# Kernel optimization log

Measured on AMD Instinct MI355X. Metric: run time of the kernel, lower is better.

Reference implementation:

```python
import jax, jax.numpy as jnp
import numpy as np

BATCH, T, HID = 4, 2048, 1024
H = P = 1024  # input_dim and ssm_size (expand_ratio=1.0)
EPS = 1e-5
DISCRETIZATION = "IM"  # 'IM' or 'IMEX'


def setup_inputs() -> dict:
    key = jax.random.key(0)
    ks = jax.random.split(key, 10)
    std_b = 1.0 / np.sqrt(H)
    std_c = 1.0 / np.sqrt(P)
    u = lambda k, s, lo, hi: jax.random.uniform(k, s, jnp.float32, lo, hi)
    return {
        "hidden_states": jax.random.normal(ks[0], (BATCH, T, HID), jnp.float32),
        "Wi": jax.random.normal(ks[1], (H, HID), jnp.float32) / np.sqrt(HID),
        "Wg": jax.random.normal(ks[2], (H, HID), jnp.float32) / np.sqrt(HID),
        "Wo": jax.random.normal(ks[3], (HID, H), jnp.float32) / np.sqrt(H),
        "A_diag": u(ks[4], (P,), 0.0, 1.0),
        "B_param": u(ks[5], (P, H, 2), -std_b, std_b),
        "C_param": u(ks[6], (H, P, 2), -std_c, std_c),
        "D": jax.random.normal(ks[7], (H,), jnp.float32),
        "dt": u(ks[8], (P,), 0.0, 1.0),
        "norm_weight": jnp.ones((H,), jnp.float32),
    }


def _linoss(x, B_param, C_param, A_diag, dt_p, D):
    """LinOSS oscillatory SSM recurrence with complex B/C and diagonal A.
    x: (B,T,H) real input. State z,y in C^P (re/im stacked on last axis)."""
    A = jax.nn.relu(A_diag)       # (P,) nonneg frequencies
    dt = jax.nn.sigmoid(dt_p)     # (P,) timesteps in (0,1)
    # Bu_{re,im}[b,t,p] = sum_h x[b,t,h] * B_{re,im}[p,h]
    Bu = jnp.einsum('bth,phc->btpc', x, B_param)  # (B,T,P,2)
    if DISCRETIZATION == "IM":
        S = 1.0 / (1.0 + dt * dt * A)
        m11, m12, m21, m22 = S, -dt * A * S, dt * S, S
        f1, f2 = dt * S, dt * dt * S
    else:  # IMEX
        one = jnp.ones_like(dt)
        m11, m12, m21, m22 = one, -dt * A, dt, 1.0 - dt * dt * A
        f1, f2 = dt, dt * dt
    c = lambda v: v[None, :, None]  # broadcast (P,) -> (B,P,2)

    def step(carry, bu):
        z, y = carry  # each (B,P,2)
        z1 = c(m11) * z + c(m12) * y + c(f1) * bu
        y1 = c(m21) * z + c(m22) * y + c(f2) * bu
        return (z1, y1), y1

    z0 = jnp.zeros((x.shape[0], A.shape[0], 2), x.dtype)
    _, ys = jax.lax.scan(step, (z0, z0), jnp.swapaxes(Bu, 0, 1))
    ys = jnp.swapaxes(ys, 0, 1)  # (B,T,P,2)
    # o = Re(C @ y) + D * x
    o = (jnp.einsum('btp,hp->bth', ys[..., 0], C_param[..., 0])
         - jnp.einsum('btp,hp->bth', ys[..., 1], C_param[..., 1]))
    return o + x * D


def reference(hidden_states, Wi, Wg, Wo, A_diag, B_param, C_param, D, dt, norm_weight):
    x = hidden_states @ Wi.T                        # i_proj
    o = _linoss(x, B_param, C_param, A_diag, dt, D)  # fused_recurrent_linoss
    g = hidden_states @ Wg.T                        # g_proj
    # FusedRMSNormGated: rmsnorm(o) * weight * swish(g)
    o = o * jax.lax.rsqrt(jnp.mean(o * o, axis=-1, keepdims=True) + EPS) * norm_weight
    o = o * (g * jax.nn.sigmoid(g))
    return o @ Wo.T                                  # o_proj
```

## Files before the change

kernel.cpp:

```cpp
#include <hip/hip_runtime.h>
#include <hip/hip_bf16.h>
#include <math.h>

#define BB 4
#define TT 2048
#define HH 1024
#define PP 1024
#define MT 8192
#define C2 2048
#define NC 64
#define LCH 32

typedef __attribute__((ext_vector_type(8))) short  bf16x8;
typedef __attribute__((ext_vector_type(4))) float  f32x4;

__device__ __forceinline__ ushort f2bf(float f) {
    union { float f; unsigned u; } v; v.f = f;
    unsigned r = v.u + 0x7fffu + ((v.u >> 16) & 1u);
    return (ushort)(r >> 16);
}
__device__ __forceinline__ float bf2f(ushort h) {
    union { unsigned u; float f; } v; v.u = ((unsigned)h) << 16;
    return v.f;
}

__device__ __forceinline__ void gload16(const ushort* g, ushort* l) {
    __builtin_amdgcn_global_load_lds((const __attribute__((address_space(1))) void*)g,
                                     (__attribute__((address_space(3))) void*)l,
                                     16, 0, 0);
}
__device__ __forceinline__ void barrier_raw() { __builtin_amdgcn_s_barrier(); }
__device__ __forceinline__ void lgk0() { asm volatile("s_waitcnt lgkmcnt(0)" ::: "memory"); }
__device__ __forceinline__ void vm6()  { asm volatile("s_waitcnt vmcnt(6)"   ::: "memory"); }
__device__ __forceinline__ void vm0()  { asm volatile("s_waitcnt vmcnt(0)"   ::: "memory"); }

__global__ void convert_all(const float* __restrict__ hs, const float* __restrict__ Wi,
                            const float* __restrict__ Wg, const float* __restrict__ Wo,
                            ushort* __restrict__ hsb, ushort* __restrict__ Wigb,
                            ushort* __restrict__ Wob) {
    int i = blockIdx.x * 256 + threadIdx.x;
    const int HS4 = MT * HH / 4;
    const int W4  = HH * HH / 4;
    const float4* s;
    ushort4* d;
    if (i < HS4)               { s = (const float4*)hs + i;               d = (ushort4*)hsb  + i; }
    else if (i < HS4 + 2 * W4) { int j = i - HS4;
                                 s = (const float4*)(j < W4 ? Wi : Wg) + (j < W4 ? j : j - W4);
                                 d = (ushort4*)Wigb + j; }
    else                       { int j = i - HS4 - 2 * W4;
                                 s = (const float4*)Wo + j;               d = (ushort4*)Wob + j; }
    float4 v = *s;
    ushort4 o;
    o.x = f2bf(v.x); o.y = f2bf(v.y); o.z = f2bf(v.z); o.w = f2bf(v.w);
    *d = o;
}

__global__ void repack_B_bf(const float* __restrict__ src, ushort* __restrict__ dst) {
    int idx = blockIdx.x * 256 + threadIdx.x;
    int p = idx >> 10;
    int h = idx & 1023;
    float2 v = ((const float2*)src)[idx];
    dst[(size_t)p * HH + h]        = f2bf(v.x);
    dst[(size_t)(p + PP) * HH + h] = f2bf(v.y);
}

__global__ void repack_C_bf(const float* __restrict__ src, ushort* __restrict__ dst) {
    int idx = blockIdx.x * 256 + threadIdx.x;
    int h = idx >> 10;
    int p = idx & 1023;
    float2 v = ((const float2*)src)[idx];
    dst[(size_t)h * C2 + p]      = f2bf(v.x);
    dst[(size_t)h * C2 + PP + p] = f2bf(-v.y);
}

template<int BM, int STORE_BF16>
__global__ __launch_bounds__(512, 2) void gemm8p(
    const ushort* __restrict__ A, int lda,
    const ushort* __restrict__ B, int ldb,
    void* __restrict__ Cp, int ldc, int K, int nbx)
{
    constexpr int BN  = 256;
    constexpr int MR  = BM / 32;
    constexpr int MRH = MR / 2;
    constexpr int TA  = BM * 128;
    constexpr int TB  = BN * 128;
    __shared__ __align__(16) char smem[2 * TA + 2 * TB];

    const int bid = blockIdx.x;
    const int cpx = gridDim.x >> 3;
    const int wg  = (bid & 7) * cpx + (bid >> 3);
    const int by  = wg / nbx;
    const int bx  = wg - by * nbx;
    const int bm  = by * BM;
    const int bn  = bx * BN;

    const int tid  = threadIdx.x;
    const int wave = tid >> 6;
    const int lane = tid & 63;
    const int wr   = wave >> 2;
    const int wc   = wave & 3;
    const int lr   = lane & 15;
    const int kg   = lane >> 4;

    const int e  = (wave << 10) + ((lane << 4) ^ (((lane >> 3) & 7) << 4));
    const int r0 = e >> 7;
    const int c0 = (e & 127) >> 1;

    auto stA = [&](int bi, int u, int kt) {
        gload16(A + (size_t)(bm + u * 64 + r0) * lda + kt * 64 + c0,
                (ushort*)(smem + bi * TA + u * 8192 + (wave << 10)));
    };
    auto stB = [&](int bi, int u, int kt) {
        gload16(B + (size_t)(bn + u * 64 + r0) * ldb + kt * 64 + c0,
                (ushort*)(smem + 2 * TA + bi * TB + u * 8192 + (wave << 10)));
    };

    bf16x8 Af[MRH][2], Bf[4][2];
    auto ldsA = [&](int bi, int qm) {
#pragma unroll
        for (int f = 0; f < MRH; ++f)
#pragma unroll
            for (int kk = 0; kk < 2; ++kk) {
                int row = wr * (BM / 2) + qm * (BM / 4) + f * 16 + lr;
                int o = row * 128 + kk * 64 + kg * 16;
                o ^= (row & 7) << 4;
                Af[f][kk] = *(const bf16x8*)(smem + bi * TA + o);
            }
    };
    auto ldsB = [&](int bi) {
#pragma unroll
        for (int n = 0; n < 4; ++n)
#pragma unroll
            for (int kk = 0; kk < 2; ++kk) {
                int row = wc * 64 + n * 16 + lr;
                int o = row * 128 + kk * 64 + kg * 16;
                o ^= (row & 7) << 4;
                Bf[n][kk] = *(const bf16x8*)(smem + 2 * TA + bi * TB + o);
            }
    };

    f32x4 acc[MR][4];
#pragma unroll
    for (int m = 0; m < MR; ++m)
#pragma unroll
        for (int n = 0; n < 4; ++n)
#pragma unroll
            for (int i = 0; i < 4; ++i) acc[m][n][i] = 0.f;

    auto mfma16 = [&](int qm, int qn) {
        __builtin_amdgcn_s_setprio(1);
#pragma unroll
        for (int f = 0; f < MRH; ++f)
#pragma unroll
            for (int n2 = 0; n2 < 2; ++n2)
#pragma unroll
                for (int kk = 0; kk < 2; ++kk)
                    acc[qm * MRH + f][qn * 2 + n2] =
                        __builtin_amdgcn_mfma_f32_16x16x32_bf16(
                            Af[f][kk], Bf[qn * 2 + n2][kk],
                            acc[qm * MRH + f][qn * 2 + n2], 0, 0, 0);
        __builtin_amdgcn_s_setprio(0);
    };

    if constexpr (BM == 256) {
        stA(0, 0, 0); stA(0, 1, 0); stA(0, 2, 0); stA(0, 3, 0);
        stB(0, 0, 0); stB(0, 1, 0); stB(0, 2, 0); stB(0, 3, 0);
        stB(1, 0, 1); stB(1, 1, 1); stB(1, 2, 1); stB(1, 3, 1);
        stA(1, 0, 1); stA(1, 2, 1);
    } else {
        stA(0, 0, 0); stA(0, 1, 0);
        stB(0, 0, 0); stB(0, 1, 0); stB(0, 2, 0); stB(0, 3, 0);
        stA(1, 0, 1); stA(1, 1, 1);
        stB(1, 0, 1); stB(1, 1, 1); stB(1, 2, 1); stB(1, 3, 1);
    }
    vm6();
    barrier_raw();

    const int nIter = K >> 7;
    for (int J = 0; J < nIter; ++J) {
        const bool pf  = (J + 1 < nIter);
        const int  kt1 = 2 * J + 1, kt2 = 2 * J + 2, kt3 = 2 * J + 3;
        ldsA(0, 0); ldsB(0);
        if constexpr (BM == 256) { stA(1, 1, kt1); stA(1, 3, kt1); }
        barrier_raw(); lgk0(); mfma16(0, 0); barrier_raw();
        if (pf) { stB(0, 0, kt2); stB(0, 1, kt2); }
        barrier_raw(); lgk0(); mfma16(0, 1); barrier_raw();
        ldsA(0, 1);
        if (pf) { stB(0, 2, kt2); stB(0, 3, kt2); }
        barrier_raw(); lgk0(); mfma16(1, 0); barrier_raw();
        if (pf) {
            if constexpr (BM == 256) { stA(0, 0, kt2); stA(0, 2, kt2); }
            else                     { stA(0, 0, kt2); stA(0, 1, kt2); }
        }
        barrier_raw(); lgk0(); mfma16(1, 1);
        if (pf) vm6(); else vm0();
        barrier_raw();
        ldsA(1, 0); ldsB(1);
        if constexpr (BM == 256) { if (pf) { stA(0, 1, kt2); stA(0, 3, kt2); } }
        barrier_raw(); lgk0(); mfma16(0, 0); barrier_raw();
        if (pf) { stB(1, 0, kt3); stB(1, 1, kt3); }
        barrier_raw(); lgk0(); mfma16(0, 1); barrier_raw();
        ldsA(1, 1);
        if (pf) { stB(1, 2, kt3); stB(1, 3, kt3); }
        barrier_raw(); lgk0(); mfma16(1, 0); barrier_raw();
        if (pf) {
            if constexpr (BM == 256) { stA(1, 0, kt3); stA(1, 2, kt3); }
            else                     { stA(1, 0, kt3); stA(1, 1, kt3); }
        }
        barrier_raw(); lgk0(); mfma16(1, 1);
        if (pf) vm6(); else vm0();
        barrier_raw();
    }

#pragma unroll
    for (int mf = 0; mf < MR; ++mf) {
#pragma unroll
        for (int n = 0; n < 4; ++n) {
            int col = bn + wc * 64 + n * 16 + lr;
#pragma unroll
            for (int i = 0; i < 4; ++i) {
                int row = bm + wr * (BM / 2) + mf * 16 + kg * 4 + i;
                float v = acc[mf][n][i];
                if (STORE_BF16)
                    ((ushort*)Cp)[(size_t)row * ldc + col] = f2bf(v);
                else
                    ((float*)Cp)[(size_t)row * ldc + col]  = v;
            }
        }
    }
}

__device__ __forceinline__ void linoss_coeffs(const float* A_diag, const float* dt_p,
                                              int p, float& m11, float& m12,
                                              float& m21, float& m22,
                                              float& f1, float& f2) {
    float A  = fmaxf(A_diag[p], 0.f);
    float dt = 1.f / (1.f + expf(-dt_p[p]));
    float S  = 1.f / (1.f + dt * dt * A);
    m11 = S;        m12 = -dt * A * S;
    m21 = dt * S;   m22 = S;
    f1  = dt * S;   f2  = dt * dt * S;
}

__global__ void scan_passA(const ushort* __restrict__ Bu,
                           const float* __restrict__ A_diag,
                           const float* __restrict__ dt_p,
                           float2* __restrict__ sEnd) {
    int c = blockIdx.x * 256 + threadIdx.x;
    int b = blockIdx.y;
    int j = blockIdx.z;
    float m11, m12, m21, m22, f1, f2;
    linoss_coeffs(A_diag, dt_p, c & 1023, m11, m12, m21, m22, f1, f2);
    const ushort* bu = Bu + ((size_t)(b * TT + j * LCH)) * C2 + c;
    float z = 0.f, y = 0.f;
#pragma unroll 8
    for (int i = 0; i < LCH; ++i) {
        float u  = bf2f(bu[(size_t)i * C2]);
        float z1 = m11 * z + m12 * y + f1 * u;
        float y1 = m21 * z + m22 * y + f2 * u;
        z = z1; y = y1;
    }
    sEnd[((size_t)j * BB + b) * C2 + c] = make_float2(z, y);
}

__global__ void scan_combine(const float* __restrict__ A_diag,
                             const float* __restrict__ dt_p,
                             const float2* __restrict__ sEnd,
                             float2* __restrict__ sInit) {
    int idx = blockIdx.x * 256 + threadIdx.x;
    int c = idx & (C2 - 1);
    int b = idx >> 11;
    float m11, m12, m21, m22, f1, f2;
    linoss_coeffs(A_diag, dt_p, c & 1023, m11, m12, m21, m22, f1, f2);
    float e11 = m11, e12 = m12, e21 = m21, e22 = m22;
#pragma unroll
    for (int s = 0; s < 5; ++s) {
        float n11 = e11 * e11 + e12 * e21;
        float n12 = e11 * e12 + e12 * e22;
        float n21 = e21 * e11 + e22 * e21;
        float n22 = e21 * e12 + e22 * e22;
        e11 = n11; e12 = n12; e21 = n21; e22 = n22;
    }
    float z = 0.f, y = 0.f;
    for (int j = 0; j < NC; ++j) {
        size_t off = ((size_t)j * BB + b) * C2 + c;
        sInit[off] = make_float2(z, y);
        float2 le = sEnd[off];
        float z1 = e11 * z + e12 * y + le.x;
        float y1 = e21 * z + e22 * y + le.y;
        z = z1; y = y1;
    }
}

__global__ void scan_passB(const ushort* __restrict__ Bu,
                           const float* __restrict__ A_diag,
                           const float* __restrict__ dt_p,
                           const float2* __restrict__ sInit,
                           ushort* __restrict__ YSb) {
    int c = blockIdx.x * 256 + threadIdx.x;
    int b = blockIdx.y;
    int j = blockIdx.z;
    float m11, m12, m21, m22, f1, f2;
    linoss_coeffs(A_diag, dt_p, c & 1023, m11, m12, m21, m22, f1, f2);
    float2 s0 = sInit[((size_t)j * BB + b) * C2 + c];
    float z = s0.x, y = s0.y;
    const ushort* bu = Bu  + ((size_t)(b * TT + j * LCH)) * C2 + c;
    ushort*       ys = YSb + ((size_t)(b * TT + j * LCH)) * C2 + c;
#pragma unroll 8
    for (int i = 0; i < LCH; ++i) {
        float u  = bf2f(bu[(size_t)i * C2]);
        float z1 = m11 * z + m12 * y + f1 * u;
        float y1 = m21 * z + m22 * y + f2 * u;
        z = z1; y = y1;
        ys[(size_t)i * C2] = f2bf(y);
    }
}

__global__ void rmsgate_kernel(const float* __restrict__ O,
                               const ushort* __restrict__ XGb,
                               const float* __restrict__ Dv,
                               const float* __restrict__ nw,
                               ushort* __restrict__ V) {
    int m = blockIdx.x;
    int t = threadIdx.x;
    float4  o4 = ((const float4*)(O + (size_t)m * HH))[t];
    ushort4 x4 = ((const ushort4*)(XGb + (size_t)m * C2))[t];
    float4  d4 = ((const float4*)Dv)[t];
    float of[4];
    of[0] = o4.x + d4.x * bf2f(x4.x);
    of[1] = o4.y + d4.y * bf2f(x4.y);
    of[2] = o4.z + d4.z * bf2f(x4.z);
    of[3] = o4.w + d4.w * bf2f(x4.w);
    float ss = of[0]*of[0] + of[1]*of[1] + of[2]*of[2] + of[3]*of[3];
#pragma unroll
    for (int o = 32; o > 0; o >>= 1) ss += __shfl_down(ss, o);
    __shared__ float wsum[4];
    if ((t & 63) == 0) wsum[t >> 6] = ss;
    __syncthreads();
    float tot = wsum[0] + wsum[1] + wsum[2] + wsum[3];
    float r = rsqrtf(tot * (1.f / (float)HH) + 1e-5f);

    ushort4 g4 = ((const ushort4*)(XGb + (size_t)m * C2 + HH))[t];
    float4  w4 = ((const float4*)nw)[t];
    float g[4] = {bf2f(g4.x), bf2f(g4.y), bf2f(g4.z), bf2f(g4.w)};
    float w[4] = {w4.x, w4.y, w4.z, w4.w};
    ushort4 vout;
    ushort* vo = &vout.x;
#pragma unroll
    for (int i = 0; i < 4; ++i) {
        float sw = g[i] / (1.f + expf(-g[i]));
        vo[i] = f2bf(of[i] * r * w[i] * sw);
    }
    ((ushort4*)(V + (size_t)m * HH))[t] = vout;
}

extern "C" void kernel_launch(void* const* d_in, const int* in_sizes, int n_in,
                              void* d_out, int out_size, void* d_ws, size_t ws_size,
                              hipStream_t stream) {
    const float* hs      = (const float*)d_in[0];
    const float* Wi      = (const float*)d_in[1];
    const float* Wg      = (const float*)d_in[2];
    const float* Wo      = (const float*)d_in[3];
    const float* A_diag  = (const float*)d_in[4];
    const float* B_param = (const float*)d_in[5];
    const float* C_param = (const float*)d_in[6];
    const float* Dv      = (const float*)d_in[7];
    const float* dtp     = (const float*)d_in[8];
    const float* nw      = (const float*)d_in[9];
    float* out = (float*)d_out;

    char* ws = (char*)d_ws;
    ushort* hsb  = (ushort*)ws;                                   ws += (size_t)MT * HH * 2;
    ushort* Wigb = (ushort*)ws;                                   ws += (size_t)C2 * HH * 2;
    ushort* Wob  = (ushort*)ws;                                   ws += (size_t)HH * HH * 2;
    ushort* Bpkb = (ushort*)ws;                                   ws += (size_t)C2 * HH * 2;
    ushort* Cpkb = (ushort*)ws;                                   ws += (size_t)HH * C2 * 2;
    ushort* XGb  = (ushort*)ws;                                   ws += (size_t)MT * C2 * 2;
    ushort* Bu   = (ushort*)ws;                                   ws += (size_t)MT * C2 * 2;
    ushort* YSb  = (ushort*)ws;                                   ws += (size_t)MT * C2 * 2;
    float*  O    = (float*)ws;                                    ws += (size_t)MT * HH * 4;
    ushort* Vb   = (ushort*)ws;                                   ws += (size_t)MT * HH * 2;
    float2* sEnd  = (float2*)ws;                                  ws += (size_t)NC * BB * C2 * 8;
    float2* sInit = (float2*)ws;

    dim3 blk(256);

    convert_all<<<dim3((MT * HH / 4 + 3 * HH * HH / 4) / 256), blk, 0, stream>>>(
        hs, Wi, Wg, Wo, hsb, Wigb, Wob);
    repack_B_bf<<<dim3((PP * HH) / 256), blk, 0, stream>>>(B_param, Bpkb);
    repack_C_bf<<<dim3((HH * PP) / 256), blk, 0, stream>>>(C_param, Cpkb);

    gemm8p<256, 1><<<dim3(256), dim3(512), 0, stream>>>(
        hsb, HH, Wigb, HH, XGb, C2, HH, 8);

    gemm8p<256, 1><<<dim3(256), dim3(512), 0, stream>>>(
        XGb, C2, Bpkb, HH, Bu, C2, HH, 8);

    scan_passA<<<dim3(C2 / 256, BB, NC), blk, 0, stream>>>(Bu, A_diag, dtp, sEnd);
    scan_combine<<<dim3((BB * C2) / 256), blk, 0, stream>>>(A_diag, dtp, sEnd, sInit);
    scan_passB<<<dim3(C2 / 256, BB, NC), blk, 0, stream>>>(Bu, A_diag, dtp, sInit, YSb);

    gemm8p<128, 0><<<dim3(256), dim3(512), 0, stream>>>(
        YSb, C2, Cpkb, C2, O, HH, C2, 4);

    rmsgate_kernel<<<dim3(MT), blk, 0, stream>>>(O, XGb, Dv, nw, Vb);

    gemm8p<128, 0><<<dim3(256), dim3(512), 0, stream>>>(
        Vb, HH, Wob, HH, out, HH, HH, 4);
}
```

Before: 196.5 us.

## Add 4-phase pipelined 128x256 GEMM for output projections and store O in bf16

```diff
diff --git a/kernel.cpp b/kernel.cpp
--- a/kernel.cpp
+++ b/kernel.cpp
@@ -31,6 +31,7 @@
 }
 __device__ __forceinline__ void barrier_raw() { __builtin_amdgcn_s_barrier(); }
 __device__ __forceinline__ void lgk0() { asm volatile("s_waitcnt lgkmcnt(0)" ::: "memory"); }
+__device__ __forceinline__ void vm4()  { asm volatile("s_waitcnt vmcnt(4)"   ::: "memory"); }
 __device__ __forceinline__ void vm6()  { asm volatile("s_waitcnt vmcnt(6)"   ::: "memory"); }
 __device__ __forceinline__ void vm0()  { asm volatile("s_waitcnt vmcnt(0)"   ::: "memory"); }
 
@@ -220,6 +221,148 @@
 #pragma unroll
             for (int i = 0; i < 4; ++i) {
                 int row = bm + wr * (BM / 2) + mf * 16 + kg * 4 + i;
+                float v = acc[mf][n][i];
+                if (STORE_BF16)
+                    ((ushort*)Cp)[(size_t)row * ldc + col] = f2bf(v);
+                else
+                    ((float*)Cp)[(size_t)row * ldc + col]  = v;
+            }
+        }
+    }
+}
+
+template<int STORE_BF16>
+__global__ __launch_bounds__(512, 2) void gemm4p(
+    const ushort* __restrict__ A, int lda,
+    const ushort* __restrict__ B, int ldb,
+    void* __restrict__ Cp, int ldc, int K, int nbx)
+{
+    constexpr int BM = 128, BN = 256;
+    constexpr int TA = BM * 128;
+    constexpr int TB = BN * 128;
+    __shared__ __align__(16) char smem[2 * TA + 2 * TB];
+
+    const int bid = blockIdx.x;
+    const int cpx = gridDim.x >> 3;
+    const int wg  = (bid & 7) * cpx + (bid >> 3);
+    const int by  = wg / nbx;
+    const int bx  = wg - by * nbx;
+    const int bm  = by * BM;
+    const int bn  = bx * BN;
+
+    const int tid  = threadIdx.x;
+    const int wave = tid >> 6;
+    const int lane = tid & 63;
+    const int wr   = wave >> 2;
+    const int wc   = wave & 3;
+    const int lr   = lane & 15;
+    const int kg   = lane >> 4;
+
+    const int e  = (wave << 10) + ((lane << 4) ^ (((lane >> 3) & 7) << 4));
+    const int r0 = e >> 7;
+    const int c0 = (e & 127) >> 1;
+
+    auto stA = [&](int bi, int u, int kt) {
+        gload16(A + (size_t)(bm + u * 64 + r0) * lda + kt * 64 + c0,
+                (ushort*)(smem + bi * TA + u * 8192 + (wave << 10)));
+    };
+    auto stB = [&](int bi, int u, int kt) {
+        gload16(B + (size_t)(bn + u * 64 + r0) * ldb + kt * 64 + c0,
+                (ushort*)(smem + 2 * TA + bi * TB + u * 8192 + (wave << 10)));
+    };
+
+    bf16x8 Af[2][2], Bf[4][2];
+    auto ldsA = [&](int bi, int qm) {
+#pragma unroll
+        for (int f = 0; f < 2; ++f)
+#pragma unroll
+            for (int kk = 0; kk < 2; ++kk) {
+                int row = wr * 64 + qm * 32 + f * 16 + lr;
+                int o = row * 128 + kk * 64 + kg * 16;
+                o ^= (row & 7) << 4;
+                Af[f][kk] = *(const bf16x8*)(smem + bi * TA + o);
+            }
+    };
+    auto ldsB = [&](int bi) {
+#pragma unroll
+        for (int n = 0; n < 4; ++n)
+#pragma unroll
+            for (int kk = 0; kk < 2; ++kk) {
+                int row = wc * 64 + n * 16 + lr;
+                int o = row * 128 + kk * 64 + kg * 16;
+                o ^= (row & 7) << 4;
+                Bf[n][kk] = *(const bf16x8*)(smem + 2 * TA + bi * TB + o);
+            }
+    };
+
+    f32x4 acc[4][4];
+#pragma unroll
+    for (int m = 0; m < 4; ++m)
+#pragma unroll
+        for (int n = 0; n < 4; ++n)
+#pragma unroll
+            for (int i = 0; i < 4; ++i) acc[m][n][i] = 0.f;
+
+    auto cl = [&](int qm) {
+        __builtin_amdgcn_s_setprio(1);
+#pragma unroll
+        for (int f = 0; f < 2; ++f)
+#pragma unroll
+            for (int n = 0; n < 4; ++n)
+#pragma unroll
+                for (int kk = 0; kk < 2; ++kk)
+                    acc[qm * 2 + f][n] =
+                        __builtin_amdgcn_mfma_f32_16x16x32_bf16(
+                            Af[f][kk], Bf[n][kk], acc[qm * 2 + f][n], 0, 0, 0);
+        __builtin_amdgcn_s_setprio(0);
+    };
+
+    stB(0, 0, 0); stB(0, 1, 0); stB(0, 2, 0); stB(0, 3, 0);
+    stA(0, 0, 0); stA(0, 1, 0);
+    stB(1, 0, 1); stB(1, 1, 1); stB(1, 2, 1); stB(1, 3, 1);
+    vm4();
+    barrier_raw();
+
+    const int nIter = K >> 7;
+    for (int J = 0; J < nIter; ++J) {
+        const bool pf  = (J + 1 < nIter);
+        const int  kt1 = 2 * J + 1, kt2 = 2 * J + 2, kt3 = 2 * J + 3;
+        ldsA(0, 0); ldsB(0);
+        stA(1, 0, kt1); stA(1, 1, kt1);
+        barrier_raw();
+        cl(0);
+        lgk0();
+        barrier_raw();
+        ldsA(0, 1);
+        if (pf) { stB(0, 0, kt2); stB(0, 1, kt2); stB(0, 2, kt2); stB(0, 3, kt2); }
+        barrier_raw();
+        cl(1);
+        lgk0();
+        if (pf) vm4(); else vm0();
+        barrier_raw();
+        ldsA(1, 0); ldsB(1);
+        if (pf) { stA(0, 0, kt2); stA(0, 1, kt2); }
+        barrier_raw();
+        cl(0);
+        lgk0();
+        barrier_raw();
+        ldsA(1, 1);
+        if (pf) { stB(1, 0, kt3); stB(1, 1, kt3); stB(1, 2, kt3); stB(1, 3, kt3); }
+        barrier_raw();
+        cl(1);
+        lgk0();
+        if (pf) vm4();
+        barrier_raw();
+    }
+
+#pragma unroll
+    for (int mf = 0; mf < 4; ++mf) {
+#pragma unroll
+        for (int n = 0; n < 4; ++n) {
+            int col = bn + wc * 64 + n * 16 + lr;
+#pragma unroll
+            for (int i = 0; i < 4; ++i) {
+                int row = bm + wr * 64 + mf * 16 + kg * 4 + i;
                 float v = acc[mf][n][i];
                 if (STORE_BF16)
                     ((ushort*)Cp)[(size_t)row * ldc + col] = f2bf(v);
@@ -316,21 +459,21 @@
     }
 }
 
-__global__ void rmsgate_kernel(const float* __restrict__ O,
+__global__ void rmsgate_kernel(const ushort* __restrict__ O,
                                const ushort* __restrict__ XGb,
                                const float* __restrict__ Dv,
                                const float* __restrict__ nw,
                                ushort* __restrict__ V) {
     int m = blockIdx.x;
     int t = threadIdx.x;
-    float4  o4 = ((const float4*)(O + (size_t)m * HH))[t];
+    ushort4 o4 = ((const ushort4*)(O + (size_t)m * HH))[t];
     ushort4 x4 = ((const ushort4*)(XGb + (size_t)m * C2))[t];
     float4  d4 = ((const float4*)Dv)[t];
     float of[4];
-    of[0] = o4.x + d4.x * bf2f(x4.x);
-    of[1] = o4.y + d4.y * bf2f(x4.y);
-    of[2] = o4.z + d4.z * bf2f(x4.z);
-    of[3] = o4.w + d4.w * bf2f(x4.w);
+    of[0] = bf2f(o4.x) + d4.x * bf2f(x4.x);
+    of[1] = bf2f(o4.y) + d4.y * bf2f(x4.y);
+    of[2] = bf2f(o4.z) + d4.z * bf2f(x4.z);
+    of[3] = bf2f(o4.w) + d4.w * bf2f(x4.w);
     float ss = of[0]*of[0] + of[1]*of[1] + of[2]*of[2] + of[3]*of[3];
 #pragma unroll
     for (int o = 32; o > 0; o >>= 1) ss += __shfl_down(ss, o);
@@ -378,7 +521,7 @@
     ushort* XGb  = (ushort*)ws;                                   ws += (size_t)MT * C2 * 2;
     ushort* Bu   = (ushort*)ws;                                   ws += (size_t)MT * C2 * 2;
     ushort* YSb  = (ushort*)ws;                                   ws += (size_t)MT * C2 * 2;
-    float*  O    = (float*)ws;                                    ws += (size_t)MT * HH * 4;
+    ushort* O    = (ushort*)ws;                                   ws += (size_t)MT * HH * 2;
     ushort* Vb   = (ushort*)ws;                                   ws += (size_t)MT * HH * 2;
     float2* sEnd  = (float2*)ws;                                  ws += (size_t)NC * BB * C2 * 8;
     float2* sInit = (float2*)ws;
@@ -400,11 +543,11 @@
     scan_combine<<<dim3((BB * C2) / 256), blk, 0, stream>>>(A_diag, dtp, sEnd, sInit);
     scan_passB<<<dim3(C2 / 256, BB, NC), blk, 0, stream>>>(Bu, A_diag, dtp, sInit, YSb);
 
-    gemm8p<128, 0><<<dim3(256), dim3(512), 0, stream>>>(
+    gemm4p<1><<<dim3(256), dim3(512), 0, stream>>>(
         YSb, C2, Cpkb, C2, O, HH, C2, 4);
 
     rmsgate_kernel<<<dim3(MT), blk, 0, stream>>>(O, XGb, Dv, nw, Vb);
 
-    gemm8p<128, 0><<<dim3(256), dim3(512), 0, stream>>>(
+    gemm4p<0><<<dim3(256), dim3(512), 0, stream>>>(
         Vb, HH, Wob, HH, out, HH, HH, 4);
 }
```

New measurement: 191.3 us. -2.7%, faster.
